# Kernel tuning notes

Measured on AMD Instinct MI355X. Metric: run time of the kernel, lower is better.

Reference implementation:

```python
import jax, jax.numpy as jnp
import numpy as np

N_CONN = 21  # n_connections


def setup_inputs() -> dict:
    key = jax.random.key(0)
    landmarks = jax.random.normal(key, (262144, N_CONN, 3), dtype=jnp.float32)
    return {"landmarks": landmarks}


def reference(landmarks) -> jnp.ndarray:
    # Faithful to the TF layer: connections = [(i, j) for i in range(n) for j in range(n)],
    # connection_vectors[k] = landmarks[:, j_k] - landmarks[:, i_k]; the loop only reads
    # indices k < n, which correspond to pairs (0, k), so v_k = p_k - p_0 (v_0 == 0).
    b, n = landmarks.shape[0], N_CONN
    v = landmarks[:, :n, :] - landmarks[:, :1, :]          # (b, n, d)
    dots = jnp.einsum("bid,bjd->bij", v, v)                 # (b, n, n)
    norms = jnp.linalg.norm(v, axis=-1)                     # (b, n)
    cos = dots / (norms[:, :, None] * norms[:, None, :])    # 0/0 -> nan for v_0
    ang = jnp.arccos(cos)                                   # (b, n, n)
    ang = jnp.where(jnp.isnan(ang), jnp.zeros_like(ang), ang)
    # TF concatenates n*n tensors of shape (batch,) along axis -1 (== axis 0),
    # yielding shape (n*n*batch,) ordered angle-major.
    return ang.reshape(b, n * n).T.reshape(-1)
```

## Files before the change

kernel.cpp:

```cpp
#include <hip/hip_runtime.h>

#define NCONN 21
#define TPB 128

__global__ __launch_bounds__(TPB) void pv_kernel(const float* __restrict__ in,
                                                 float* __restrict__ out,
                                                 int B) {
    __shared__ float lds[TPB * 63];
    const int tid = threadIdx.x;
    const long long blockBatch = (long long)blockIdx.x * TPB;

    const long long gBase  = blockBatch * 63;
    const long long totalF4 = ((long long)B * 63) >> 2;
    const float4* in4 = (const float4*)in;
    const long long gBase4 = gBase >> 2;
    float4* lds4 = (float4*)lds;
    #pragma unroll
    for (int it = 0; it < 16; ++it) {
        int t = tid + it * TPB;
        if (t < (TPB * 63) / 4) {
            long long g4 = gBase4 + t;
            if (g4 < totalF4) lds4[t] = in4[g4];
        }
    }
    __syncthreads();

    const long long bl = blockBatch + tid;
    if (bl >= B) return;
    const int b = (int)bl;
    float* base = lds + tid * 63;

    const float p0x = base[0], p0y = base[1], p0z = base[2];
    #pragma unroll
    for (int e = 1; e < NCONN; ++e) {
        float vx = base[3*e+0] - p0x;
        float vy = base[3*e+1] - p0y;
        float vz = base[3*e+2] - p0z;
        float d  = fmaf(vx, vx, fmaf(vy, vy, vz * vz));
        float r  = rsqrtf(d);
        base[3*e+0] = vx * r;
        base[3*e+1] = vy * r;
        base[3*e+2] = vz * r;
    }

    const size_t sB = (size_t)B;
    float* outb = out + b;

    #pragma unroll
    for (int k = 0; k < NCONN; ++k) outb[(size_t)k * sB] = 0.0f;

    #pragma unroll
    for (int cc = 0; cc < 2; ++cc) {
        const int i0 = 1 + cc * 10;
        float uix[10], uiy[10], uiz[10];
        #pragma unroll
        for (int q = 0; q < 10; ++q) {
            uix[q] = base[3*(i0+q)+0];
            uiy[q] = base[3*(i0+q)+1];
            uiz[q] = base[3*(i0+q)+2];
        }
        #pragma unroll
        for (int q = 0; q < 10; ++q)
            outb[(size_t)((i0+q)*NCONN) * sB] = 0.0f;

        for (int j = 1; j < NCONN; ++j) {
            const float ujx = base[3*j+0];
            const float ujy = base[3*j+1];
            const float ujz = base[3*j+2];
            #pragma unroll
            for (int q = 0; q < 10; ++q) {
                float c = fmaf(uix[q], ujx, fmaf(uiy[q], ujy, uiz[q] * ujz));
                c = fmaxf(fminf(c, 1.0f), -1.0f);
                float t = fabsf(c);
                float s = sqrtf(1.0f - t);
                float p = fmaf(t, -0.0187293f, 0.0742610f);
                p = fmaf(t, p, -0.2121144f);
                p = fmaf(t, p, 1.5707288f);
                float r = s * p;
                float ang = (c >= 0.0f) ? r : (3.14159265358979f - r);
                outb[(size_t)((i0+q)*NCONN + j) * sB] = ang;
            }
        }
    }
}

extern "C" void kernel_launch(void* const* d_in, const int* in_sizes, int n_in,
                              void* d_out, int out_size, void* d_ws, size_t ws_size,
                              hipStream_t stream) {
    const float* in = (const float*)d_in[0];
    float* out = (float*)d_out;
    const int B = in_sizes[0] / (NCONN * 3);
    const int grid = (B + TPB - 1) / TPB;
    hipLaunchKernelGGL(pv_kernel, dim3(grid), dim3(TPB), 0, stream, in, out, B);
}
```

Before: 529.7 us.

## Stage angle rows in LDS tile and write out with coalesced float4 stores

Each thread now computes one row of 21 angles at a time into a shared-memory tile, and the block then writes the tile to global memory with float4 stores. This replaces the per-thread scalar stores spread across the output. Bounds checks are dropped and the grid becomes B/TPB, so the kernel assumes B is a multiple of 128. The change adds two barriers per row and more LDS traffic.

```diff
diff --git a/kernel.cpp b/kernel.cpp
--- a/kernel.cpp
+++ b/kernel.cpp
@@ -6,70 +6,47 @@
 __global__ __launch_bounds__(TPB) void pv_kernel(const float* __restrict__ in,
                                                  float* __restrict__ out,
                                                  int B) {
-    __shared__ float lds[TPB * 63];
+    __shared__ float u[TPB * 63];
+    __shared__ float tile[NCONN * TPB];
     const int tid = threadIdx.x;
     const long long blockBatch = (long long)blockIdx.x * TPB;
 
-    const long long gBase  = blockBatch * 63;
-    const long long totalF4 = ((long long)B * 63) >> 2;
-    const float4* in4 = (const float4*)in;
-    const long long gBase4 = gBase >> 2;
-    float4* lds4 = (float4*)lds;
+    const float4* in4 = (const float4*)in + ((blockBatch * 63) >> 2);
+    float4* u4 = (float4*)u;
     #pragma unroll
     for (int it = 0; it < 16; ++it) {
         int t = tid + it * TPB;
-        if (t < (TPB * 63) / 4) {
-            long long g4 = gBase4 + t;
-            if (g4 < totalF4) lds4[t] = in4[g4];
-        }
+        if (t < (TPB * 63) / 4) u4[t] = in4[t];
     }
     __syncthreads();
 
-    const long long bl = blockBatch + tid;
-    if (bl >= B) return;
-    const int b = (int)bl;
-    float* base = lds + tid * 63;
-
+    float* base = u + tid * 63;
     const float p0x = base[0], p0y = base[1], p0z = base[2];
     #pragma unroll
     for (int e = 1; e < NCONN; ++e) {
         float vx = base[3*e+0] - p0x;
         float vy = base[3*e+1] - p0y;
         float vz = base[3*e+2] - p0z;
-        float d  = fmaf(vx, vx, fmaf(vy, vy, vz * vz));
-        float r  = rsqrtf(d);
+        float r  = rsqrtf(fmaf(vx, vx, fmaf(vy, vy, vz * vz)));
         base[3*e+0] = vx * r;
         base[3*e+1] = vy * r;
         base[3*e+2] = vz * r;
     }
 
     const size_t sB = (size_t)B;
-    float* outb = out + b;
+    float* outBlock = out + blockBatch;
 
-    #pragma unroll
-    for (int k = 0; k < NCONN; ++k) outb[(size_t)k * sB] = 0.0f;
-
-    #pragma unroll
-    for (int cc = 0; cc < 2; ++cc) {
-        const int i0 = 1 + cc * 10;
-        float uix[10], uiy[10], uiz[10];
-        #pragma unroll
-        for (int q = 0; q < 10; ++q) {
-            uix[q] = base[3*(i0+q)+0];
-            uiy[q] = base[3*(i0+q)+1];
-            uiz[q] = base[3*(i0+q)+2];
-        }
-        #pragma unroll
-        for (int q = 0; q < 10; ++q)
-            outb[(size_t)((i0+q)*NCONN) * sB] = 0.0f;
-
-        for (int j = 1; j < NCONN; ++j) {
-            const float ujx = base[3*j+0];
-            const float ujy = base[3*j+1];
-            const float ujz = base[3*j+2];
+    for (int i = 0; i < NCONN; ++i) {
+        if (i == 0) {
             #pragma unroll
-            for (int q = 0; q < 10; ++q) {
-                float c = fmaf(uix[q], ujx, fmaf(uiy[q], ujy, uiz[q] * ujz));
+            for (int j = 0; j < NCONN; ++j) tile[j * TPB + tid] = 0.0f;
+        } else {
+            const float uix = base[3*i+0], uiy = base[3*i+1], uiz = base[3*i+2];
+            tile[tid] = 0.0f;
+            #pragma unroll 4
+            for (int j = 1; j < NCONN; ++j) {
+                float c = fmaf(uix, base[3*j+0],
+                         fmaf(uiy, base[3*j+1], uiz * base[3*j+2]));
                 c = fmaxf(fminf(c, 1.0f), -1.0f);
                 float t = fabsf(c);
                 float s = sqrtf(1.0f - t);
@@ -77,10 +54,23 @@
                 p = fmaf(t, p, -0.2121144f);
                 p = fmaf(t, p, 1.5707288f);
                 float r = s * p;
-                float ang = (c >= 0.0f) ? r : (3.14159265358979f - r);
-                outb[(size_t)((i0+q)*NCONN + j) * sB] = ang;
+                tile[j * TPB + tid] = (c >= 0.0f) ? r : (3.14159265358979f - r);
             }
         }
+        __syncthreads();
+
+        const float4* t4 = (const float4*)tile;
+        #pragma unroll
+        for (int it = 0; it < 6; ++it) {
+            int v = tid + it * TPB;
+            if (v < NCONN * (TPB / 4)) {
+                int row = v >> 5;
+                int q   = v & 31;
+                float4 val = t4[row * (TPB / 4) + q];
+                *(float4*)(outBlock + (size_t)(i * NCONN + row) * sB + 4 * q) = val;
+            }
+        }
+        __syncthreads();
     }
 }
 
@@ -90,6 +80,6 @@
     const float* in = (const float*)d_in[0];
     float* out = (float*)d_out;
     const int B = in_sizes[0] / (NCONN * 3);
-    const int grid = (B + TPB - 1) / TPB;
+    const int grid = B / TPB;
     hipLaunchKernelGGL(pv_kernel, dim3(grid), dim3(TPB), 0, stream, in, out, B);
 }
```

Measured after the change: 578.3 us. +9.2%, slower.
